# Optimization experiments

Measured on AMD Instinct MI355X. Metric: run time of the kernel, lower is better.

## Reference

```python
import jax, jax.numpy as jnp
import numpy as np

B, T, C = 4, 4096, 128

def setup_inputs() -> dict:
    key = jax.random.key(0)
    k1, k2, k3, k4 = jax.random.split(key, 4)
    x = jax.random.normal(k1, (B, T, C), dtype=jnp.float32)
    s = 1.0 / np.sqrt(C)
    Wq = jax.random.normal(k2, (C, C), dtype=jnp.float32) * s
    Wk = jax.random.normal(k3, (C, C), dtype=jnp.float32) * s
    Wv = jax.random.normal(k4, (C, C), dtype=jnp.float32) * s
    return {"x": x, "Wq": Wq, "Wk": Wk, "Wv": Wv}

def reference(x, Wq, Wk, Wv):
    # nn.Linear(bias=False): y = x @ W.T
    q = jnp.einsum('btc,dc->btd', x, Wq)
    k = jnp.einsum('btc,dc->btd', x, Wk)
    v = jnp.einsum('btc,dc->btd', x, Wv)
    scale = 1.0 / jnp.sqrt(jnp.asarray(x.shape[-1], x.dtype))
    att = jnp.einsum('btd,bsd->bts', q, k) * scale  # [B,T,T]
    causal = jnp.tril(jnp.ones((x.shape[1], x.shape[1]), dtype=bool))
    att = jnp.where(causal[None, :, :], att, -jnp.inf)
    w = jax.nn.softmax(att, axis=-1)
    # dropout p=0.0 -> identity
    out = jnp.einsum('bts,bsd->btd', w, v)
    return out
```

## Files before the change

kernel.cpp:

```cpp
#include <hip/hip_runtime.h>
#include <hip/hip_bf16.h>
#include <math.h>

#define T_SEQ 4096
#define C_DIM 128
#define B_SZ  4

typedef __attribute__((ext_vector_type(8))) short short8;
typedef __attribute__((ext_vector_type(4))) short short4v;
typedef __attribute__((ext_vector_type(4))) float f32x4;

__device__ __forceinline__ short f2bf(float f) {
    union { float fv; unsigned u; } v; v.fv = f;
    unsigned r = v.u + 0x7fff + ((v.u >> 16) & 1);
    return (short)(r >> 16);
}

__device__ __forceinline__ unsigned pk_bf16(float a, float b) {
    union { __hip_bfloat162 h2; unsigned u; } c;
    c.h2 = __float22bfloat162_rn(make_float2(a, b));
    return c.u;
}

__device__ __forceinline__ short8 load_f32x8_bf16(const float* p) {
    const float4* q = (const float4*)p;
    float4 a = q[0], b = q[1];
    short8 r;
    r[0] = f2bf(a.x); r[1] = f2bf(a.y); r[2] = f2bf(a.z); r[3] = f2bf(a.w);
    r[4] = f2bf(b.x); r[5] = f2bf(b.y); r[6] = f2bf(b.z); r[7] = f2bf(b.w);
    return r;
}

__device__ __forceinline__ void async_cp16(const short* g, short* l) {
    __builtin_amdgcn_global_load_lds(
        (const __attribute__((address_space(1))) unsigned int*)g,
        (__attribute__((address_space(3))) unsigned int*)l, 16, 0, 0);
}

__global__ __launch_bounds__(512) void qkv_proj(
    const float* __restrict__ x, const float* __restrict__ Wq,
    const float* __restrict__ Wk, const float* __restrict__ Wv,
    short* __restrict__ Q, short* __restrict__ Kf, short* __restrict__ Vf)
{
    __shared__ short8 Wl[2048];

    const int tid  = threadIdx.x;
    const int lane = tid & 63;
    const int ln15 = lane & 15;
    const int quad = lane >> 4;
    const int mat  = blockIdx.x >> 6;
    const int rt   = (blockIdx.x & 63) * 8 + (tid >> 6);
    const int m0   = rt * 32;

    const float* W = (mat == 0) ? Wq : (mat == 1) ? Wk : Wv;

    for (int i = tid; i < 2048; i += 512) {
        int n = i >> 4, kc = i & 15;
        short8 v = load_f32x8_bf16(W + n * C_DIM + kc * 8);
        Wl[((n >> 4) * 4 + (kc >> 2)) * 64 + (kc & 3) * 16 + (n & 15)] = v;
    }

    short8 afr[2][4];
#pragma unroll
    for (int ms = 0; ms < 2; ++ms) {
        const float* xrow = x + (size_t)(m0 + ms * 16 + ln15) * C_DIM + quad * 8;
#pragma unroll
        for (int ks = 0; ks < 4; ++ks)
            afr[ms][ks] = load_f32x8_bf16(xrow + ks * 32);
    }

    __syncthreads();

    const float scale = (mat == 0) ? (0.08838834764831845f * 1.4426950408889634f)
                                   : 1.0f;
    const int b  = m0 >> 12;
    const int tl = m0 & 4095;

#pragma unroll
    for (int nt = 0; nt < 8; ++nt) {
        f32x4 acc0 = {0.f, 0.f, 0.f, 0.f};
        f32x4 acc1 = {0.f, 0.f, 0.f, 0.f};
#pragma unroll
        for (int ks = 0; ks < 4; ++ks) {
            short8 bfr = Wl[(nt * 4 + ks) * 64 + lane];
            if (mat == 2) {
                acc0 = __builtin_amdgcn_mfma_f32_16x16x32_bf16(afr[0][ks], bfr, acc0, 0, 0, 0);
                acc1 = __builtin_amdgcn_mfma_f32_16x16x32_bf16(afr[1][ks], bfr, acc1, 0, 0, 0);
            } else {
                acc0 = __builtin_amdgcn_mfma_f32_16x16x32_bf16(bfr, afr[0][ks], acc0, 0, 0, 0);
                acc1 = __builtin_amdgcn_mfma_f32_16x16x32_bf16(bfr, afr[1][ks], acc1, 0, 0, 0);
            }
        }
        if (mat == 0) {
            short4v s0, s1;
#pragma unroll
            for (int r = 0; r < 4; ++r) { s0[r] = f2bf(acc0[r] * scale); s1[r] = f2bf(acc1[r] * scale); }
            *(short4v*)&Q[(size_t)(m0 + ln15) * C_DIM + nt * 16 + quad * 4]      = s0;
            *(short4v*)&Q[(size_t)(m0 + 16 + ln15) * C_DIM + nt * 16 + quad * 4] = s1;
        } else if (mat == 1) {
            short4v s0, s1;
#pragma unroll
            for (int r = 0; r < 4; ++r) { s0[r] = f2bf(acc0[r]); s1[r] = f2bf(acc1[r]); }
            const int ks     = nt >> 1;
            const int quad_k = (nt & 1) * 2 + (quad >> 1);
            const int j0     = (quad & 1) * 4;
            {
                const int A0 = (tl >> 4) & 3;
                const int rd = tl >> 6;
                const int kt = (A0 >> 1) * 2 + ((ln15 >> 2) & 1);
                const int ar = (((A0 & 1) << 1) | ((ln15 >> 3) & 1)) * 4 + (ln15 & 3);
                size_t a = ((size_t)b << 19) + (size_t)rd * 8192
                         + (kt * 4 + ks) * 512 + quad_k * 128 + ar * 8 + j0;
                *(short4v*)&Kf[a] = s0;
            }
            {
                const int A1 = ((tl >> 4) + 1) & 3;
                const int rd = (tl + 16) >> 6;
                const int kt = (A1 >> 1) * 2 + ((ln15 >> 2) & 1);
                const int ar = (((A1 & 1) << 1) | ((ln15 >> 3) & 1)) * 4 + (ln15 & 3);
                size_t a = ((size_t)b << 19) + (size_t)rd * 8192
                         + (kt * 4 + ks) * 512 + quad_k * 128 + ar * 8 + j0;
                *(short4v*)&Kf[a] = s1;
            }
        } else {
            const int kvc = tl >> 5;
            short4v s0, s1;
#pragma unroll
            for (int r = 0; r < 4; ++r) { s0[r] = f2bf(acc0[r]); s1[r] = f2bf(acc1[r]); }
            short* vbase = Vf + (((size_t)(b * 128 + kvc) * 8 + nt) << 9);
            *(short4v*)&vbase[((quad >> 1) * 16 + ln15) * 8 + (quad & 1) * 4]       = s0;
            *(short4v*)&vbase[(((quad >> 1) + 2) * 16 + ln15) * 8 + (quad & 1) * 4] = s1;
        }
    }
}


#define ROUND_BODY(KC, VC, KN, VN, R)                                        \
  {                                                                          \
    const int kv0 = (R) << 7;                                                \
     \
    asm volatile("s_waitcnt vmcnt(0)" ::: "memory");                         \
    __builtin_amdgcn_sched_barrier(0);                                       \
    __builtin_amdgcn_s_barrier();                                            \
    __builtin_amdgcn_sched_barrier(0);                                       \
    if ((R) + 1 <= kmax) {                                                   \
      const short* gk = Kb + (size_t)((R) + 1) * 16384 + w * 2048;           \
      const short* gv = Vb + (size_t)((R) + 1) * 16384 + w * 2048;           \
      _Pragma("unroll")                                                      \
      for (int i = 0; i < 4; ++i) {                                          \
        async_cp16(gk + i * 512 + lane * 8, &KN[w * 2048 + i * 512]);        \
        async_cp16(gv + i * 512 + lane * 8, &VN[w * 2048 + i * 512]);        \
      }                                                                      \
    }                                                                        \
          \
    f32x4 St0 = {0.f, 0.f, 0.f, 0.f}, St1 = {0.f, 0.f, 0.f, 0.f};            \
    _Pragma("unroll")                                                        \
    for (int ks = 0; ks < 4; ++ks) {                                         \
      short8 k0 = *(const short8*)&KC[sq * 4096 + ks * 512 + lane * 8];      \
      short8 k1 = *(const short8*)&KC[sq * 4096 + 2048 + ks * 512 + lane*8]; \
      St0 = __builtin_amdgcn_mfma_f32_16x16x32_bf16(k0, qf[ks], St0, 0,0,0); \
      St1 = __builtin_amdgcn_mfma_f32_16x16x32_bf16(k1, qf[ks], St1, 0,0,0); \
    }                                                                        \
      \
    if (kv0 + sq * 32 + 31 > q0w) {                                          \
      const int qcol = q0w + ln15;                                           \
      const int kb   = kv0 + sq * 32 + quad * 8;                             \
      _Pragma("unroll")                                                      \
      for (int rr = 0; rr < 4; ++rr) {                                       \
        if (kb + rr > qcol)     St0[rr] = -INFINITY;                         \
        if (kb + 4 + rr > qcol) St1[rr] = -INFINITY;                         \
      }                                                                      \
    }                                                                        \
     \
    union { unsigned u[4]; short8 s8; } pa;                                  \
    {                                                                        \
      float p0 = __builtin_amdgcn_exp2f(St0[0] - 16.f);                      \
      float p1 = __builtin_amdgcn_exp2f(St0[1] - 16.f);                      \
      float p2 = __builtin_amdgcn_exp2f(St0[2] - 16.f);                      \
      float p3 = __builtin_amdgcn_exp2f(St0[3] - 16.f);                      \
      float p4 = __builtin_amdgcn_exp2f(St1[0] - 16.f);                      \
      float p5 = __builtin_amdgcn_exp2f(St1[1] - 16.f);                      \
      float p6 = __builtin_amdgcn_exp2f(St1[2] - 16.f);                      \
      float p7 = __builtin_amdgcn_exp2f(St1[3] - 16.f);                      \
      l_i += ((p0 + p1) + (p2 + p3)) + ((p4 + p5) + (p6 + p7));              \
      pa.u[0] = pk_bf16(p0, p1);                                             \
      pa.u[1] = pk_bf16(p2, p3);                                             \
      pa.u[2] = pk_bf16(p4, p5);                                             \
      pa.u[3] = pk_bf16(p6, p7);                                             \
    }                                                                        \
                        \
    _Pragma("unroll")                                                        \
    for (int dt = 0; dt < 8; ++dt) {                                         \
      short8 vfr = *(const short8*)&VC[(sq * 8 + dt) * 512 + lane * 8];      \
      acc[dt] = __builtin_amdgcn_mfma_f32_16x16x32_bf16(pa.s8, vfr,          \
                                                        acc[dt], 0, 0, 0);   \
    }                                                                        \
  }

__global__ __launch_bounds__(512, 2) void flash_attn(
    const short* __restrict__ Q, const short* __restrict__ Kf,
    const short* __restrict__ Vf, float* __restrict__ out)
{
    __shared__ short Klds0[16384];
    __shared__ short Klds1[16384];
    __shared__ short Vlds0[16384];
    __shared__ short Vlds1[16384];
    __shared__ float lsf[2][16];

    const int tid  = threadIdx.x;
    const int w    = tid >> 6;
    const int lane = tid & 63;
    const int ln15 = lane & 15;
    const int quad = lane >> 4;
    const int qh   = w >> 2;
    const int sq   = w & 3;
    const int bid  = blockIdx.x;
    const int b    = bid & 3;
    const int pi   = bid >> 2;

    const short* Qb = Q  + ((size_t)b << 19);
    const short* Kb = Kf + ((size_t)b << 19);
    const short* Vb = Vf + ((size_t)b << 19);
    float* outb = out + ((size_t)b << 19);

    for (int half = 0; half < 2; ++half) {
        const int c    = half ? (127 - pi) : pi;
        const int q0   = c * 32;
        const int q0w  = q0 + qh * 16;
        const int kmax = (q0 + 31) >> 7;

        short8 qf[4];
        {
            const short* qrow = Qb + (size_t)(q0w + ln15) * C_DIM + quad * 8;
#pragma unroll
            for (int ks = 0; ks < 4; ++ks)
                qf[ks] = *(const short8*)(qrow + ks * 32);
        }

        f32x4 acc[8];
#pragma unroll
        for (int dt = 0; dt < 8; ++dt)
            acc[dt] = (f32x4){0.f, 0.f, 0.f, 0.f};
        float l_i = 0.f;

        {
            const short* gk = Kb + w * 2048;
            const short* gv = Vb + w * 2048;
#pragma unroll
            for (int i = 0; i < 4; ++i) {
                async_cp16(gk + i * 512 + lane * 8, &Klds0[w * 2048 + i * 512]);
                async_cp16(gv + i * 512 + lane * 8, &Vlds0[w * 2048 + i * 512]);
            }
        }

        int r = 0;
        while (true) {
            ROUND_BODY(Klds0, Vlds0, Klds1, Vlds1, r);
            if (++r > kmax) break;
            ROUND_BODY(Klds1, Vlds1, Klds0, Vlds0, r);
            if (++r > kmax) break;
        }

        __syncthreads();
        if (tid < 32) ((float*)lsf)[tid] = 0.f;
        __syncthreads();
        atomicAdd(&lsf[qh][ln15], l_i);
        {
            f32x4* ex = (f32x4*)(qh == 0 ? Klds0 : Vlds0);
#pragma unroll
            for (int dt = 0; dt < 8; ++dt)
                ex[(sq * 8 + dt) * 64 + lane] = acc[dt];
        }
        __syncthreads();

        {
            const f32x4* ex = (const f32x4*)(qh == 0 ? Klds0 : Vlds0);
            float li[4];
#pragma unroll
            for (int reg = 0; reg < 4; ++reg)
                li[reg] = 1.0f / lsf[qh][quad * 4 + reg];

            const int row0 = q0w + quad * 4;
#pragma unroll
            for (int dd = 0; dd < 2; ++dd) {
                const int dt = sq * 2 + dd;
                f32x4 sum = ex[(0 * 8 + dt) * 64 + lane];
#pragma unroll
                for (int sq2 = 1; sq2 < 4; ++sq2) {
                    f32x4 p = ex[(sq2 * 8 + dt) * 64 + lane];
#pragma unroll
                    for (int reg = 0; reg < 4; ++reg) sum[reg] += p[reg];
                }
                const int col = dt * 16 + ln15;
#pragma unroll
                for (int reg = 0; reg < 4; ++reg)
                    outb[(size_t)(row0 + reg) * C_DIM + col] =
                        sum[reg] * li[reg];
            }
        }
        __syncthreads();
    }
}

extern "C" void kernel_launch(void* const* d_in, const int* in_sizes, int n_in,
                              void* d_out, int out_size, void* d_ws, size_t ws_size,
                              hipStream_t stream) {
    const float* x  = (const float*)d_in[0];
    const float* Wq = (const float*)d_in[1];
    const float* Wk = (const float*)d_in[2];
    const float* Wv = (const float*)d_in[3];
    float* out = (float*)d_out;

    const size_t elems = (size_t)B_SZ * T_SEQ * C_DIM;
    short* Q  = (short*)d_ws;
    short* Kf = Q  + elems;
    short* Vf = Kf + elems;

    hipLaunchKernelGGL(qkv_proj, dim3(192), dim3(512), 0, stream,
                       x, Wq, Wk, Wv, Q, Kf, Vf);
    hipLaunchKernelGGL(flash_attn, dim3(256), dim3(512), 0, stream,
                       Q, Kf, Vf, out);
}
```

Measured before the change: 121.1 us.

## Split KV across all 8 waves with register-prefetched K/V instead of LDS

```diff
diff --git a/kernel.cpp b/kernel.cpp
--- a/kernel.cpp
+++ b/kernel.cpp
@@ -29,12 +29,6 @@
     r[0] = f2bf(a.x); r[1] = f2bf(a.y); r[2] = f2bf(a.z); r[3] = f2bf(a.w);
     r[4] = f2bf(b.x); r[5] = f2bf(b.y); r[6] = f2bf(b.z); r[7] = f2bf(b.w);
     return r;
-}
-
-__device__ __forceinline__ void async_cp16(const short* g, short* l) {
-    __builtin_amdgcn_global_load_lds(
-        (const __attribute__((address_space(1))) unsigned int*)g,
-        (__attribute__((address_space(3))) unsigned int*)l, 16, 0, 0);
 }
 
 __global__ __launch_bounds__(512) void qkv_proj(
@@ -135,65 +129,68 @@
 }
 
 
-#define ROUND_BODY(KC, VC, KN, VN, R)                                        \
+#define UNIT(KR, KN, I)                                                      \
   {                                                                          \
-    const int kv0 = (R) << 7;                                                \
-     \
-    asm volatile("s_waitcnt vmcnt(0)" ::: "memory");                         \
-    __builtin_amdgcn_sched_barrier(0);                                       \
-    __builtin_amdgcn_s_barrier();                                            \
-    __builtin_amdgcn_sched_barrier(0);                                       \
-    if ((R) + 1 <= kmax) {                                                   \
-      const short* gk = Kb + (size_t)((R) + 1) * 16384 + w * 2048;           \
-      const short* gv = Vb + (size_t)((R) + 1) * 16384 + w * 2048;           \
-      _Pragma("unroll")                                                      \
-      for (int i = 0; i < 4; ++i) {                                          \
-        async_cp16(gk + i * 512 + lane * 8, &KN[w * 2048 + i * 512]);        \
-        async_cp16(gv + i * 512 + lane * 8, &VN[w * 2048 + i * 512]);        \
-      }                                                                      \
-    }                                                                        \
-          \
-    f32x4 St0 = {0.f, 0.f, 0.f, 0.f}, St1 = {0.f, 0.f, 0.f, 0.f};            \
+    f32x4 S0a = {0.f,0.f,0.f,0.f}, S0b = {0.f,0.f,0.f,0.f};                  \
+    f32x4 S1a = {0.f,0.f,0.f,0.f}, S1b = {0.f,0.f,0.f,0.f};                  \
     _Pragma("unroll")                                                        \
     for (int ks = 0; ks < 4; ++ks) {                                         \
-      short8 k0 = *(const short8*)&KC[sq * 4096 + ks * 512 + lane * 8];      \
-      short8 k1 = *(const short8*)&KC[sq * 4096 + 2048 + ks * 512 + lane*8]; \
-      St0 = __builtin_amdgcn_mfma_f32_16x16x32_bf16(k0, qf[ks], St0, 0,0,0); \
-      St1 = __builtin_amdgcn_mfma_f32_16x16x32_bf16(k1, qf[ks], St1, 0,0,0); \
-    }                                                                        \
-      \
-    if (kv0 + sq * 32 + 31 > q0w) {                                          \
-      const int qcol = q0w + ln15;                                           \
-      const int kb   = kv0 + sq * 32 + quad * 8;                             \
+      S0a = __builtin_amdgcn_mfma_f32_16x16x32_bf16(KR[ks],   qf0[ks], S0a, 0,0,0); \
+      S0b = __builtin_amdgcn_mfma_f32_16x16x32_bf16(KR[4+ks], qf0[ks], S0b, 0,0,0); \
+      S1a = __builtin_amdgcn_mfma_f32_16x16x32_bf16(KR[ks],   qf1[ks], S1a, 0,0,0); \
+      S1b = __builtin_amdgcn_mfma_f32_16x16x32_bf16(KR[4+ks], qf1[ks], S1b, 0,0,0); \
+    }                                                                        \
+    const int nx = (I) + 8;                                                  \
+    if (nx <= c) {             \
+      const short* kp = Kb + (size_t)nx * 4096;                              \
+      _Pragma("unroll")                                                      \
+      for (int j = 0; j < 8; ++j)                                            \
+        KN[j] = *(const short8*)(kp + j * 512 + lane * 8);                   \
+    }                                                                        \
+    if ((I) == c) {             \
       _Pragma("unroll")                                                      \
       for (int rr = 0; rr < 4; ++rr) {                                       \
-        if (kb + rr > qcol)     St0[rr] = -INFINITY;                         \
-        if (kb + 4 + rr > qcol) St1[rr] = -INFINITY;                         \
+        if (quad * 8 + rr > ln15)          S0a[rr] = -INFINITY;              \
+        if (quad * 8 + 4 + rr > ln15)      S0b[rr] = -INFINITY;              \
+        if (quad * 8 + rr > 16 + ln15)     S1a[rr] = -INFINITY;              \
+        if (quad * 8 + 4 + rr > 16 + ln15) S1b[rr] = -INFINITY;              \
       }                                                                      \
     }                                                                        \
-     \
-    union { unsigned u[4]; short8 s8; } pa;                                  \
+    union { unsigned u[4]; short8 s8; } pa0, pa1;                            \
     {                                                                        \
-      float p0 = __builtin_amdgcn_exp2f(St0[0] - 16.f);                      \
-      float p1 = __builtin_amdgcn_exp2f(St0[1] - 16.f);                      \
-      float p2 = __builtin_amdgcn_exp2f(St0[2] - 16.f);                      \
-      float p3 = __builtin_amdgcn_exp2f(St0[3] - 16.f);                      \
-      float p4 = __builtin_amdgcn_exp2f(St1[0] - 16.f);                      \
-      float p5 = __builtin_amdgcn_exp2f(St1[1] - 16.f);                      \
-      float p6 = __builtin_amdgcn_exp2f(St1[2] - 16.f);                      \
-      float p7 = __builtin_amdgcn_exp2f(St1[3] - 16.f);                      \
-      l_i += ((p0 + p1) + (p2 + p3)) + ((p4 + p5) + (p6 + p7));              \
-      pa.u[0] = pk_bf16(p0, p1);                                             \
-      pa.u[1] = pk_bf16(p2, p3);                                             \
-      pa.u[2] = pk_bf16(p4, p5);                                             \
-      pa.u[3] = pk_bf16(p6, p7);                                             \
-    }                                                                        \
-                        \
+      float p0 = __builtin_amdgcn_exp2f(S0a[0] - 16.f);                      \
+      float p1 = __builtin_amdgcn_exp2f(S0a[1] - 16.f);                      \
+      float p2 = __builtin_amdgcn_exp2f(S0a[2] - 16.f);                      \
+      float p3 = __builtin_amdgcn_exp2f(S0a[3] - 16.f);                      \
+      float p4 = __builtin_amdgcn_exp2f(S0b[0] - 16.f);                      \
+      float p5 = __builtin_amdgcn_exp2f(S0b[1] - 16.f);                      \
+      float p6 = __builtin_amdgcn_exp2f(S0b[2] - 16.f);                      \
+      float p7 = __builtin_amdgcn_exp2f(S0b[3] - 16.f);                      \
+      l0 += ((p0 + p1) + (p2 + p3)) + ((p4 + p5) + (p6 + p7));               \
+      pa0.u[0] = pk_bf16(p0, p1); pa0.u[1] = pk_bf16(p2, p3);                \
+      pa0.u[2] = pk_bf16(p4, p5); pa0.u[3] = pk_bf16(p6, p7);                \
+      float r0 = __builtin_amdgcn_exp2f(S1a[0] - 16.f);                      \
+      float r1 = __builtin_amdgcn_exp2f(S1a[1] - 16.f);                      \
+      float r2 = __builtin_amdgcn_exp2f(S1a[2] - 16.f);                      \
+      float r3 = __builtin_amdgcn_exp2f(S1a[3] - 16.f);                      \
+      float r4 = __builtin_amdgcn_exp2f(S1b[0] - 16.f);                      \
+      float r5 = __builtin_amdgcn_exp2f(S1b[1] - 16.f);                      \
+      float r6 = __builtin_amdgcn_exp2f(S1b[2] - 16.f);                      \
+      float r7 = __builtin_amdgcn_exp2f(S1b[3] - 16.f);                      \
+      l1 += ((r0 + r1) + (r2 + r3)) + ((r4 + r5) + (r6 + r7));               \
+      pa1.u[0] = pk_bf16(r0, r1); pa1.u[1] = pk_bf16(r2, r3);                \
+      pa1.u[2] = pk_bf16(r4, r5); pa1.u[3] = pk_bf16(r6, r7);                \
+    }                                                                        \
     _Pragma("unroll")                                                        \
     for (int dt = 0; dt < 8; ++dt) {                                         \
-      short8 vfr = *(const short8*)&VC[(sq * 8 + dt) * 512 + lane * 8];      \
-      acc[dt] = __builtin_amdgcn_mfma_f32_16x16x32_bf16(pa.s8, vfr,          \
-                                                        acc[dt], 0, 0, 0);   \
+      acc0[dt] = __builtin_amdgcn_mfma_f32_16x16x32_bf16(pa0.s8, va[dt], acc0[dt], 0,0,0); \
+      acc1[dt] = __builtin_amdgcn_mfma_f32_16x16x32_bf16(pa1.s8, va[dt], acc1[dt], 0,0,0); \
+    }                                                                        \
+    if (nx <= c) {               \
+      const short* vp = Vb + (size_t)nx * 4096;                              \
+      _Pragma("unroll")                                                      \
+      for (int j = 0; j < 8; ++j)                                            \
+        va[j] = *(const short8*)(vp + j * 512 + lane * 8);                   \
     }                                                                        \
   }
 
@@ -201,19 +198,14 @@
     const short* __restrict__ Q, const short* __restrict__ Kf,
     const short* __restrict__ Vf, float* __restrict__ out)
 {
-    __shared__ short Klds0[16384];
-    __shared__ short Klds1[16384];
-    __shared__ short Vlds0[16384];
-    __shared__ short Vlds1[16384];
-    __shared__ float lsf[2][16];
+    __shared__ f32x4 ex[8][16][64];
+    __shared__ float lsf[2][2][16];
 
     const int tid  = threadIdx.x;
     const int w    = tid >> 6;
     const int lane = tid & 63;
     const int ln15 = lane & 15;
     const int quad = lane >> 4;
-    const int qh   = w >> 2;
-    const int sq   = w & 3;
     const int bid  = blockIdx.x;
     const int b    = bid & 3;
     const int pi   = bid >> 2;
@@ -223,82 +215,76 @@
     const short* Vb = Vf + ((size_t)b << 19);
     float* outb = out + ((size_t)b << 19);
 
+    if (tid < 64) ((float*)lsf)[tid] = 0.f;
+
     for (int half = 0; half < 2; ++half) {
-        const int c    = half ? (127 - pi) : pi;
-        const int q0   = c * 32;
-        const int q0w  = q0 + qh * 16;
-        const int kmax = (q0 + 31) >> 7;
-
-        short8 qf[4];
+        const int c  = half ? (127 - pi) : pi;
+        const int q0 = c * 32;
+
+        short8 qf0[4], qf1[4];
         {
-            const short* qrow = Qb + (size_t)(q0w + ln15) * C_DIM + quad * 8;
-#pragma unroll
-            for (int ks = 0; ks < 4; ++ks)
-                qf[ks] = *(const short8*)(qrow + ks * 32);
-        }
-
-        f32x4 acc[8];
-#pragma unroll
-        for (int dt = 0; dt < 8; ++dt)
-            acc[dt] = (f32x4){0.f, 0.f, 0.f, 0.f};
-        float l_i = 0.f;
-
-        {
-            const short* gk = Kb + w * 2048;
-            const short* gv = Vb + w * 2048;
-#pragma unroll
-            for (int i = 0; i < 4; ++i) {
-                async_cp16(gk + i * 512 + lane * 8, &Klds0[w * 2048 + i * 512]);
-                async_cp16(gv + i * 512 + lane * 8, &Vlds0[w * 2048 + i * 512]);
-            }
-        }
-
-        int r = 0;
-        while (true) {
-            ROUND_BODY(Klds0, Vlds0, Klds1, Vlds1, r);
-            if (++r > kmax) break;
-            ROUND_BODY(Klds1, Vlds1, Klds0, Vlds0, r);
-            if (++r > kmax) break;
+            const short* q0r = Qb + (size_t)(q0 + ln15) * C_DIM + quad * 8;
+            const short* q1r = Qb + (size_t)(q0 + 16 + ln15) * C_DIM + quad * 8;
+#pragma unroll
+            for (int ks = 0; ks < 4; ++ks) {
+                qf0[ks] = *(const short8*)(q0r + ks * 32);
+                qf1[ks] = *(const short8*)(q1r + ks * 32);
+            }
+        }
+
+        f32x4 acc0[8], acc1[8];
+#pragma unroll
+        for (int dt = 0; dt < 8; ++dt) {
+            acc0[dt] = (f32x4){0.f, 0.f, 0.f, 0.f};
+            acc1[dt] = (f32x4){0.f, 0.f, 0.f, 0.f};
+        }
+        float l0 = 0.f, l1 = 0.f;
+
+        short8 kra[8], krb[8], va[8];
+        int i = w;
+        if (i <= c) {
+            const short* kp = Kb + (size_t)i * 4096;
+            const short* vp = Vb + (size_t)i * 4096;
+#pragma unroll
+            for (int j = 0; j < 8; ++j) {
+                kra[j] = *(const short8*)(kp + j * 512 + lane * 8);
+                va[j]  = *(const short8*)(vp + j * 512 + lane * 8);
+            }
+        }
+        while (i <= c) {
+            UNIT(kra, krb, i);
+            i += 8;
+            if (i > c) break;
+            UNIT(krb, kra, i);
+            i += 8;
         }
 
         __syncthreads();
-        if (tid < 32) ((float*)lsf)[tid] = 0.f;
+        atomicAdd(&lsf[half][0][ln15], l0);
+        atomicAdd(&lsf[half][1][ln15], l1);
+#pragma unroll
+        for (int dt = 0; dt < 8; ++dt) {
+            ex[w][dt][lane]     = acc0[dt];
+            ex[w][8 + dt][lane] = acc1[dt];
+        }
         __syncthreads();
-        atomicAdd(&lsf[qh][ln15], l_i);
-        {
-            f32x4* ex = (f32x4*)(qh == 0 ? Klds0 : Vlds0);
-#pragma unroll
-            for (int dt = 0; dt < 8; ++dt)
-                ex[(sq * 8 + dt) * 64 + lane] = acc[dt];
-        }
-        __syncthreads();
-
-        {
-            const f32x4* ex = (const f32x4*)(qh == 0 ? Klds0 : Vlds0);
-            float li[4];
-#pragma unroll
-            for (int reg = 0; reg < 4; ++reg)
-                li[reg] = 1.0f / lsf[qh][quad * 4 + reg];
-
-            const int row0 = q0w + quad * 4;
-#pragma unroll
-            for (int dd = 0; dd < 2; ++dd) {
-                const int dt = sq * 2 + dd;
-                f32x4 sum = ex[(0 * 8 + dt) * 64 + lane];
-#pragma unroll
-                for (int sq2 = 1; sq2 < 4; ++sq2) {
-                    f32x4 p = ex[(sq2 * 8 + dt) * 64 + lane];
-#pragma unroll
-                    for (int reg = 0; reg < 4; ++reg) sum[reg] += p[reg];
-                }
-                const int col = dt * 16 + ln15;
-#pragma unroll
-                for (int reg = 0; reg < 4; ++reg)
-                    outb[(size_t)(row0 + reg) * C_DIM + col] =
-                        sum[reg] * li[reg];
-            }
-        }
-        __syncthreads();
+#pragma unroll
+        for (int pp = 0; pp < 2; ++pp) {
+            const int pidx = w * 2 + pp;
+            const int qt = pidx >> 3, dt = pidx & 7;
+            f32x4 s = ex[0][pidx][lane];
+#pragma unroll
+            for (int s2 = 1; s2 < 8; ++s2) {
+                f32x4 t = ex[s2][pidx][lane];
+                s[0] += t[0]; s[1] += t[1]; s[2] += t[2]; s[3] += t[3];
+            }
+            const int row0 = q0 + qt * 16 + quad * 4;
+            const int col  = dt * 16 + ln15;
+#pragma unroll
+            for (int rr = 0; rr < 4; ++rr)
+                outb[(size_t)(row0 + rr) * C_DIM + col] =
+                    s[rr] * (1.0f / lsf[half][qt][quad * 4 + rr]);
+        }
     }
 }
 
```

Result: slower. 273.5 us (+125.8%).

## Split attention KV range across four blocks with separate combine kernel

Applied to the files above, without the earlier changes.

```diff
diff --git a/kernel.cpp b/kernel.cpp
--- a/kernel.cpp
+++ b/kernel.cpp
@@ -37,7 +37,7 @@
         (__attribute__((address_space(3))) unsigned int*)l, 16, 0, 0);
 }
 
-__global__ __launch_bounds__(512) void qkv_proj(
+__global__ __launch_bounds__(256) void qkv_proj(
     const float* __restrict__ x, const float* __restrict__ Wq,
     const float* __restrict__ Wk, const float* __restrict__ Wv,
     short* __restrict__ Q, short* __restrict__ Kf, short* __restrict__ Vf)
@@ -48,13 +48,15 @@
     const int lane = tid & 63;
     const int ln15 = lane & 15;
     const int quad = lane >> 4;
-    const int mat  = blockIdx.x >> 6;
-    const int rt   = (blockIdx.x & 63) * 8 + (tid >> 6);
+    const int mat  = blockIdx.x >> 7;
+    const int rt   = (blockIdx.x & 127) * 4 + (tid >> 6);
     const int m0   = rt * 32;
 
     const float* W = (mat == 0) ? Wq : (mat == 1) ? Wk : Wv;
 
-    for (int i = tid; i < 2048; i += 512) {
+#pragma unroll
+    for (int it = 0; it < 8; ++it) {
+        int i = tid + it * 256;
         int n = i >> 4, kc = i & 15;
         short8 v = load_f32x8_bf16(W + n * C_DIM + kc * 8);
         Wl[((n >> 4) * 4 + (kc >> 2)) * 64 + (kc & 3) * 16 + (n & 15)] = v;
@@ -135,170 +137,181 @@
 }
 
 
-#define ROUND_BODY(KC, VC, KN, VN, R)                                        \
+#define CHUNK(KB_, VB_, S, T)                                                \
+  if ((T) <= gg) {                                                           \
+    const int cc = qq + 4 * (T);                                             \
+    if (32 * cc <= Rw + 15) {                                                \
+      short8 kfr[8];                                                         \
+      _Pragma("unroll")                                                      \
+      for (int j = 0; j < 8; ++j)                                            \
+        kfr[j] = *(const short8*)&(KB_)[(S) * 4096 + j * 512 + lane * 8];    \
+      f32x4 Sa = {0.f,0.f,0.f,0.f}, Sb = {0.f,0.f,0.f,0.f};                  \
+      _Pragma("unroll")                                                      \
+      for (int ks = 0; ks < 4; ++ks) {                                       \
+        Sa = __builtin_amdgcn_mfma_f32_16x16x32_bf16(kfr[ks],   qf[ks], Sa, 0,0,0); \
+        Sb = __builtin_amdgcn_mfma_f32_16x16x32_bf16(kfr[4+ks], qf[ks], Sb, 0,0,0); \
+      }                                                                      \
+      if (32 * cc + 31 > Rw) {                                               \
+        const int qcol = Rw + ln15;                                          \
+        const int kb   = 32 * cc + quad * 8;                                 \
+        _Pragma("unroll")                                                    \
+        for (int rr = 0; rr < 4; ++rr) {                                     \
+          if (kb + rr > qcol)     Sa[rr] = -INFINITY;                        \
+          if (kb + 4 + rr > qcol) Sb[rr] = -INFINITY;                        \
+        }                                                                    \
+      }                                                                      \
+      union { unsigned u[4]; short8 s8; } pa;                                \
+      {                                                                      \
+        float p0 = __builtin_amdgcn_exp2f(Sa[0] - 16.f);                     \
+        float p1 = __builtin_amdgcn_exp2f(Sa[1] - 16.f);                     \
+        float p2 = __builtin_amdgcn_exp2f(Sa[2] - 16.f);                     \
+        float p3 = __builtin_amdgcn_exp2f(Sa[3] - 16.f);                     \
+        float p4 = __builtin_amdgcn_exp2f(Sb[0] - 16.f);                     \
+        float p5 = __builtin_amdgcn_exp2f(Sb[1] - 16.f);                     \
+        float p6 = __builtin_amdgcn_exp2f(Sb[2] - 16.f);                     \
+        float p7 = __builtin_amdgcn_exp2f(Sb[3] - 16.f);                     \
+        l_i += ((p0 + p1) + (p2 + p3)) + ((p4 + p5) + (p6 + p7));            \
+        pa.u[0] = pk_bf16(p0, p1); pa.u[1] = pk_bf16(p2, p3);                \
+        pa.u[2] = pk_bf16(p4, p5); pa.u[3] = pk_bf16(p6, p7);                \
+      }                                                                      \
+      _Pragma("unroll")                                                      \
+      for (int dt = 0; dt < 8; ++dt) {                                       \
+        short8 vfr = *(const short8*)&(VB_)[(S) * 4096 + dt * 512 + lane * 8]; \
+        acc[dt] = __builtin_amdgcn_mfma_f32_16x16x32_bf16(pa.s8, vfr,        \
+                                                          acc[dt], 0, 0, 0); \
+      }                                                                      \
+    }                                                                        \
+  }
+
+#define ROUND(KC, VC, KN, VN, R)                                             \
   {                                                                          \
-    const int kv0 = (R) << 7;                                                \
-     \
+                            \
     asm volatile("s_waitcnt vmcnt(0)" ::: "memory");                         \
     __builtin_amdgcn_sched_barrier(0);                                       \
     __builtin_amdgcn_s_barrier();                                            \
     __builtin_amdgcn_sched_barrier(0);                                       \
-    if ((R) + 1 <= kmax) {                                                   \
-      const short* gk = Kb + (size_t)((R) + 1) * 16384 + w * 2048;           \
-      const short* gv = Vb + (size_t)((R) + 1) * 16384 + w * 2048;           \
-      _Pragma("unroll")                                                      \
-      for (int i = 0; i < 4; ++i) {                                          \
-        async_cp16(gk + i * 512 + lane * 8, &KN[w * 2048 + i * 512]);        \
-        async_cp16(gv + i * 512 + lane * 8, &VN[w * 2048 + i * 512]);        \
+          \
+    {                                                                        \
+      const int slot = (w >> 1) & 1;                                         \
+      const int tS   = 2 * (R) + 2 + slot;                                   \
+      if (tS <= gg) {                                                        \
+        const int hw = w & 1;                                                \
+        const short* src = ((w < 4) ? Kb : Vb)                               \
+                         + (size_t)(qq + 4 * tS) * 4096 + hw * 2048;         \
+        short* dst = ((w < 4) ? (KN) : (VN)) + slot * 4096 + hw * 2048;      \
+        _Pragma("unroll")                                                    \
+        for (int i = 0; i < 4; ++i)                                          \
+          async_cp16(src + i * 512 + lane * 8, dst + i * 512);               \
       }                                                                      \
     }                                                                        \
-          \
-    f32x4 St0 = {0.f, 0.f, 0.f, 0.f}, St1 = {0.f, 0.f, 0.f, 0.f};            \
-    _Pragma("unroll")                                                        \
-    for (int ks = 0; ks < 4; ++ks) {                                         \
-      short8 k0 = *(const short8*)&KC[sq * 4096 + ks * 512 + lane * 8];      \
-      short8 k1 = *(const short8*)&KC[sq * 4096 + 2048 + ks * 512 + lane*8]; \
-      St0 = __builtin_amdgcn_mfma_f32_16x16x32_bf16(k0, qf[ks], St0, 0,0,0); \
-      St1 = __builtin_amdgcn_mfma_f32_16x16x32_bf16(k1, qf[ks], St1, 0,0,0); \
-    }                                                                        \
-      \
-    if (kv0 + sq * 32 + 31 > q0w) {                                          \
-      const int qcol = q0w + ln15;                                           \
-      const int kb   = kv0 + sq * 32 + quad * 8;                             \
-      _Pragma("unroll")                                                      \
-      for (int rr = 0; rr < 4; ++rr) {                                       \
-        if (kb + rr > qcol)     St0[rr] = -INFINITY;                         \
-        if (kb + 4 + rr > qcol) St1[rr] = -INFINITY;                         \
-      }                                                                      \
-    }                                                                        \
-     \
-    union { unsigned u[4]; short8 s8; } pa;                                  \
-    {                                                                        \
-      float p0 = __builtin_amdgcn_exp2f(St0[0] - 16.f);                      \
-      float p1 = __builtin_amdgcn_exp2f(St0[1] - 16.f);                      \
-      float p2 = __builtin_amdgcn_exp2f(St0[2] - 16.f);                      \
-      float p3 = __builtin_amdgcn_exp2f(St0[3] - 16.f);                      \
-      float p4 = __builtin_amdgcn_exp2f(St1[0] - 16.f);                      \
-      float p5 = __builtin_amdgcn_exp2f(St1[1] - 16.f);                      \
-      float p6 = __builtin_amdgcn_exp2f(St1[2] - 16.f);                      \
-      float p7 = __builtin_amdgcn_exp2f(St1[3] - 16.f);                      \
-      l_i += ((p0 + p1) + (p2 + p3)) + ((p4 + p5) + (p6 + p7));              \
-      pa.u[0] = pk_bf16(p0, p1);                                             \
-      pa.u[1] = pk_bf16(p2, p3);                                             \
-      pa.u[2] = pk_bf16(p4, p5);                                             \
-      pa.u[3] = pk_bf16(p6, p7);                                             \
-    }                                                                        \
-                        \
-    _Pragma("unroll")                                                        \
-    for (int dt = 0; dt < 8; ++dt) {                                         \
-      short8 vfr = *(const short8*)&VC[(sq * 8 + dt) * 512 + lane * 8];      \
-      acc[dt] = __builtin_amdgcn_mfma_f32_16x16x32_bf16(pa.s8, vfr,          \
-                                                        acc[dt], 0, 0, 0);   \
-    }                                                                        \
+    CHUNK(KC, VC, 0, 2 * (R))                                                \
+    CHUNK(KC, VC, 1, 2 * (R) + 1)                                            \
   }
 
 __global__ __launch_bounds__(512, 2) void flash_attn(
     const short* __restrict__ Q, const short* __restrict__ Kf,
-    const short* __restrict__ Vf, float* __restrict__ out)
+    const short* __restrict__ Vf, float* __restrict__ part,
+    float* __restrict__ lpart)
 {
-    __shared__ short Klds0[16384];
-    __shared__ short Klds1[16384];
-    __shared__ short Vlds0[16384];
-    __shared__ short Vlds1[16384];
-    __shared__ float lsf[2][16];
+    __shared__ short Kld0[8192];
+    __shared__ short Kld1[8192];
+    __shared__ short Vld0[8192];
+    __shared__ short Vld1[8192];
 
     const int tid  = threadIdx.x;
     const int w    = tid >> 6;
     const int lane = tid & 63;
     const int ln15 = lane & 15;
     const int quad = lane >> 4;
-    const int qh   = w >> 2;
-    const int sq   = w & 3;
     const int bid  = blockIdx.x;
-    const int b    = bid & 3;
-    const int pi   = bid >> 2;
+    const int gg   = 31 - (bid >> 4);
+    const int b    = (bid >> 2) & 3;
+    const int qq   = bid & 3;
+
+    const int Rw   = 128 * gg + 16 * w;
+    const int nrounds = (gg >> 1) + 1;
 
     const short* Qb = Q  + ((size_t)b << 19);
     const short* Kb = Kf + ((size_t)b << 19);
     const short* Vb = Vf + ((size_t)b << 19);
-    float* outb = out + ((size_t)b << 19);
-
-    for (int half = 0; half < 2; ++half) {
-        const int c    = half ? (127 - pi) : pi;
-        const int q0   = c * 32;
-        const int q0w  = q0 + qh * 16;
-        const int kmax = (q0 + 31) >> 7;
-
-        short8 qf[4];
-        {
-            const short* qrow = Qb + (size_t)(q0w + ln15) * C_DIM + quad * 8;
-#pragma unroll
-            for (int ks = 0; ks < 4; ++ks)
-                qf[ks] = *(const short8*)(qrow + ks * 32);
+
+    short8 qf[4];
+    {
+        const short* qrow = Qb + (size_t)(Rw + ln15) * C_DIM + quad * 8;
+#pragma unroll
+        for (int ks = 0; ks < 4; ++ks)
+            qf[ks] = *(const short8*)(qrow + ks * 32);
+    }
+
+    f32x4 acc[8];
+#pragma unroll
+    for (int dt = 0; dt < 8; ++dt)
+        acc[dt] = (f32x4){0.f, 0.f, 0.f, 0.f};
+    float l_i = 0.f;
+
+    {
+        const int slot = (w >> 1) & 1;
+        const int tS   = slot;
+        if (tS <= gg) {
+            const int hw = w & 1;
+            const short* src = ((w < 4) ? Kb : Vb)
+                             + (size_t)(qq + 4 * tS) * 4096 + hw * 2048;
+            short* dst = ((w < 4) ? Kld0 : Vld0) + slot * 4096 + hw * 2048;
+#pragma unroll
+            for (int i = 0; i < 4; ++i)
+                async_cp16(src + i * 512 + lane * 8, dst + i * 512);
         }
-
-        f32x4 acc[8];
-#pragma unroll
-        for (int dt = 0; dt < 8; ++dt)
-            acc[dt] = (f32x4){0.f, 0.f, 0.f, 0.f};
-        float l_i = 0.f;
-
-        {
-            const short* gk = Kb + w * 2048;
-            const short* gv = Vb + w * 2048;
-#pragma unroll
-            for (int i = 0; i < 4; ++i) {
-                async_cp16(gk + i * 512 + lane * 8, &Klds0[w * 2048 + i * 512]);
-                async_cp16(gv + i * 512 + lane * 8, &Vlds0[w * 2048 + i * 512]);
-            }
+    }
+
+    int r = 0;
+    while (true) {
+        ROUND(Kld0, Vld0, Kld1, Vld1, r);
+        if (++r >= nrounds) break;
+        ROUND(Kld1, Vld1, Kld0, Vld0, r);
+        if (++r >= nrounds) break;
+    }
+
+    l_i += __shfl_xor(l_i, 16);
+    l_i += __shfl_xor(l_i, 32);
+
+    float* pp = part + (((size_t)(qq * 4 + b)) * 4096 + Rw) * 128;
+#pragma unroll
+    for (int dt = 0; dt < 8; ++dt)
+#pragma unroll
+        for (int rr = 0; rr < 4; ++rr)
+            pp[(quad * 4 + rr) * 128 + dt * 16 + ln15] = acc[dt][rr];
+    if (quad == 0)
+        lpart[(size_t)(qq * 4 + b) * 4096 + Rw + ln15] = l_i;
+}
+
+__global__ __launch_bounds__(256) void combine(
+    const float* __restrict__ part, const float* __restrict__ lpart,
+    float* __restrict__ out)
+{
+    const int tid = threadIdx.x;
+    const int bid = blockIdx.x;
+
+#pragma unroll
+    for (int i = 0; i < 8; ++i) {
+        int f4  = bid * 2048 + i * 256 + tid;
+        int c4  = f4 & 31;
+        int row = f4 >> 5;
+        int b   = row >> 12;
+        int trow = row & 4095;
+
+        float4 p = make_float4(0.f, 0.f, 0.f, 0.f);
+        float  l = 0.f;
+#pragma unroll
+        for (int q = 0; q < 4; ++q) {
+            size_t base = (((size_t)(q * 4 + b)) * 4096 + trow) * 128 + c4 * 4;
+            float4 pq = *(const float4*)&part[base];
+            p.x += pq.x; p.y += pq.y; p.z += pq.z; p.w += pq.w;
+            l += lpart[(size_t)(q * 4 + b) * 4096 + trow];
         }
-
-        int r = 0;
-        while (true) {
-            ROUND_BODY(Klds0, Vlds0, Klds1, Vlds1, r);
-            if (++r > kmax) break;
-            ROUND_BODY(Klds1, Vlds1, Klds0, Vlds0, r);
-            if (++r > kmax) break;
-        }
-
-        __syncthreads();
-        if (tid < 32) ((float*)lsf)[tid] = 0.f;
-        __syncthreads();
-        atomicAdd(&lsf[qh][ln15], l_i);
-        {
-            f32x4* ex = (f32x4*)(qh == 0 ? Klds0 : Vlds0);
-#pragma unroll
-            for (int dt = 0; dt < 8; ++dt)
-                ex[(sq * 8 + dt) * 64 + lane] = acc[dt];
-        }
-        __syncthreads();
-
-        {
-            const f32x4* ex = (const f32x4*)(qh == 0 ? Klds0 : Vlds0);
-            float li[4];
-#pragma unroll
-            for (int reg = 0; reg < 4; ++reg)
-                li[reg] = 1.0f / lsf[qh][quad * 4 + reg];
-
-            const int row0 = q0w + quad * 4;
-#pragma unroll
-            for (int dd = 0; dd < 2; ++dd) {
-                const int dt = sq * 2 + dd;
-                f32x4 sum = ex[(0 * 8 + dt) * 64 + lane];
-#pragma unroll
-                for (int sq2 = 1; sq2 < 4; ++sq2) {
-                    f32x4 p = ex[(sq2 * 8 + dt) * 64 + lane];
-#pragma unroll
-                    for (int reg = 0; reg < 4; ++reg) sum[reg] += p[reg];
-                }
-                const int col = dt * 16 + ln15;
-#pragma unroll
-                for (int reg = 0; reg < 4; ++reg)
-                    outb[(size_t)(row0 + reg) * C_DIM + col] =
-                        sum[reg] * li[reg];
-            }
-        }
-        __syncthreads();
+        float li = 1.0f / l;
+        float4 v;
+        v.x = p.x * li; v.y = p.y * li; v.z = p.z * li; v.w = p.w * li;
+        ((float4*)out)[f4] = v;
     }
 }
 
@@ -315,9 +328,13 @@
     short* Q  = (short*)d_ws;
     short* Kf = Q  + elems;
     short* Vf = Kf + elems;
-
-    hipLaunchKernelGGL(qkv_proj, dim3(192), dim3(512), 0, stream,
+    float* part  = (float*)(Vf + elems);
+    float* lpart = part + (size_t)16 * 4096 * 128;
+
+    hipLaunchKernelGGL(qkv_proj, dim3(384), dim3(256), 0, stream,
                        x, Wq, Wk, Wv, Q, Kf, Vf);
-    hipLaunchKernelGGL(flash_attn, dim3(256), dim3(512), 0, stream,
-                       Q, Kf, Vf, out);
-}
+    hipLaunchKernelGGL(flash_attn, dim3(512), dim3(512), 0, stream,
+                       Q, Kf, Vf, part, lpart);
+    hipLaunchKernelGGL(combine, dim3(256), dim3(256), 0, stream,
+                       part, lpart, out);
+}
```

After: 109.3 us. -9.8%, faster.
